# Kernel optimization log

Hardware: AMD Instinct MI355X
Metric: run time of the kernel (lower is better)

## Reference

```python
import jax, jax.numpy as jnp
import numpy as np

B, L, H, V, HALF = 128, 4096, 64, 64, 32
ALPHA = 0.95
LN_EPS = 1e-5


def _normalize(x):
    # torch F.normalize(dim=-1): x / max(||x||_2, 1e-12)
    n = jnp.linalg.norm(x, axis=-1, keepdims=True)
    return x / jnp.maximum(n, 1e-12)


def setup_inputs() -> dict:
    key = jax.random.key(0)
    ks = jax.random.split(key, 17)
    s = 0.05
    return {
        "seq": jax.random.randint(ks[0], (B, L), 0, V),
        "embed": jax.random.normal(ks[1], (V, H), jnp.float32),
        "W1": jax.random.normal(ks[2], (H, 2 * H), jnp.float32) * s,
        "b1": jnp.zeros((2 * H,), jnp.float32),
        "W2": jax.random.normal(ks[3], (2 * H, H), jnp.float32) * s,
        "b2": jnp.zeros((H,), jnp.float32),
        "gamma": jnp.ones((H,), jnp.float32),
        "beta": jnp.zeros((H,), jnp.float32),
        "Ws": jax.random.normal(ks[4], (H, HALF), jnp.float32) * s,
        "bs": jnp.zeros((HALF,), jnp.float32),
        "We": jax.random.normal(ks[5], (H, HALF), jnp.float32) * s,
        "be": jnp.zeros((HALF,), jnp.float32),
        "Wrp": jax.random.normal(ks[6], (2 * HALF, H), jnp.float32) * s,
        "brp": jnp.zeros((H,), jnp.float32),
        "Wout": jax.random.normal(ks[7], (H, V), jnp.float32) * s,
        "bout": jnp.zeros((V,), jnp.float32),
    }


def _forward(seq, embed, W1, b1, W2, b2, gamma, beta,
             Ws, bs, We, be, Wrp, brp, Wout, bout):
    # Encoder: embed + FF(ReLU) residual + LayerNorm
    h0 = embed[seq]                                   # [B,L,H]
    ff = jnp.maximum(h0 @ W1 + b1, 0.0) @ W2 + b2
    x = h0 + ff
    mu = x.mean(-1, keepdims=True)
    var = ((x - mu) ** 2).mean(-1, keepdims=True)
    h = (x - mu) / jnp.sqrt(var + LN_EPS) * gamma + beta  # [B,L,H]

    # Precompute per-step projections for t = 0 .. L-2
    hp = h[:, :-1, :]                                 # [B,L-1,H]
    hs = hp @ Ws + bs                                 # [B,L-1,HALF]
    he = hp @ We + be
    ksn = _normalize(hs)
    ken = _normalize(he)
    scale = (jnp.arange(L - 1, dtype=h.dtype) + 1.0) / L  # (t+1)/L

    def step(carry, inp):
        M_s, M_e = carry                              # [B,HALF,HALF]
        hs_t, he_t, ks_t, ke_t, sc = inp
        vps = jnp.einsum('bij,bj->bi', M_s, ks_t)
        vpe = jnp.einsum('bij,bj->bi', M_e, ke_t)
        M_s = M_s + (1.0 - ALPHA) * (hs_t - vps)[:, :, None] * ks_t[:, None, :]
        M_e = M_e + (1.0 - ALPHA) * sc * (he_t - vpe)[:, :, None] * ke_t[:, None, :]
        return (M_s, M_e), None

    xs = (jnp.swapaxes(hs, 0, 1), jnp.swapaxes(he, 0, 1),
          jnp.swapaxes(ksn, 0, 1), jnp.swapaxes(ken, 0, 1), scale)
    M0 = jnp.zeros((B, HALF, HALF), h.dtype)
    (M_s, M_e), _ = jax.lax.scan(step, (M0, M0), xs)

    # Read with last-token query
    q = h[:, -1, :]
    qs = _normalize(q @ Ws + bs)
    qe = _normalize(q @ We + be)
    rs = jnp.einsum('bij,bj->bi', M_s, qs)
    re = jnp.einsum('bij,bj->bi', M_e, qe)
    r = jnp.concatenate([rs, re], axis=-1)            # [B,2*HALF]
    return (r @ Wrp + brp) @ Wout + bout              # [B,V]


def reference(seq, embed, W1, b1, W2, b2, gamma, beta,
              Ws, bs, We, be, Wrp, brp, Wout, bout):
    return _forward(seq, embed, W1, b1, W2, b2, gamma, beta,
                    Ws, bs, We, be, Wrp, brp, Wout, bout)
```

## Files before the change

kernel.cpp:

```cpp
#include <hip/hip_runtime.h>
#include <hip/hip_bf16.h>
#include <stdint.h>


#define BETA 0.05f
#define NB 128
#define NL 4096
#define TC 16
#define NCH 256
#define NBLD 7
#define SLOT_F 1360
#define NSLOT 14

#define L_GR   (NSLOT * SLOT_F)
#define L_DA   (L_GR + 4096)
#define L_RV   (L_DA + 64)
#define L_O1   (L_RV + 64)
#define L_WHO  (L_O1 + 64)
#define L_TOT  (L_WHO + 1)

struct Ptrs { const void* p[15]; };

__device__ inline float readlane_f(float v, int l) {
    return __int_as_float(__builtin_amdgcn_readlane(__float_as_int(v), l));
}
__device__ inline float ldT(const float* p, int i) { return p[i]; }
__device__ inline float ldT(const __hip_bfloat16* p, int i) { return __bfloat162float(p[i]); }

template <typename T>
__device__ void build_tables_body(const T* emb, const T* W1, const T* b1,
                                  const T* W2, const T* b2, const T* gam,
                                  const T* bet, const T* Wsm, const T* bsv,
                                  const T* Wem, const T* bev, float* tbl)
{
    int v = blockIdx.x;
    int j = threadIdx.x;
    __shared__ float h0s[64];
    __shared__ float act[128];
    __shared__ float hrow[64];

    float h0 = ldT(emb, v * 64 + j);
    h0s[j] = h0;
    __syncthreads();

    float za = ldT(b1, j);
    float zb = ldT(b1, j + 64);
    for (int k = 0; k < 64; ++k) {
        float hk = h0s[k];
        za = fmaf(hk, ldT(W1, k * 128 + j), za);
        zb = fmaf(hk, ldT(W1, k * 128 + j + 64), zb);
    }
    act[j] = fmaxf(za, 0.0f);
    act[j + 64] = fmaxf(zb, 0.0f);
    __syncthreads();

    float ff = ldT(b2, j);
    for (int k = 0; k < 128; ++k)
        ff = fmaf(act[k], ldT(W2, k * 64 + j), ff);
    float x = h0 + ff;

    float s = x;
    for (int off = 32; off >= 1; off >>= 1) s += __shfl_xor(s, off, 64);
    float mu = s * (1.0f / 64.0f);
    float d = x - mu;
    float s2 = d * d;
    for (int off = 32; off >= 1; off >>= 1) s2 += __shfl_xor(s2, off, 64);
    float var = s2 * (1.0f / 64.0f);
    float h = d / sqrtf(var + 1e-5f) * ldT(gam, j) + ldT(bet, j);
    hrow[j] = h;
    __syncthreads();

    if (j < 32) {
        float sv = ldT(bsv, j);
        for (int k = 0; k < 64; ++k)
            sv = fmaf(hrow[k], ldT(Wsm, k * 32 + j), sv);
        float n2 = sv * sv;
        for (int off = 16; off >= 1; off >>= 1) n2 += __shfl_xor(n2, off, 64);
        float nrm = fmaxf(sqrtf(n2), 1e-12f);
        tbl[v * 32 + j] = sv;
        tbl[2048 + v * 32 + j] = sv / nrm;
    } else {
        int jj = j - 32;
        float ev = ldT(bev, jj);
        for (int k = 0; k < 64; ++k)
            ev = fmaf(hrow[k], ldT(Wem, k * 32 + jj), ev);
        float n2 = ev * ev;
        for (int off = 16; off >= 1; off >>= 1) n2 += __shfl_xor(n2, off, 64);
        float nrm = fmaxf(sqrtf(n2), 1e-12f);
        tbl[4096 + v * 32 + jj] = ev;
        tbl[6144 + v * 32 + jj] = ev / nrm;
    }
}

__global__ __launch_bounds__(64, 2) void build_tables(Ptrs ps, float* __restrict__ tbl,
                                                      int* __restrict__ flags)
{
    if (blockIdx.x == 0) {
        flags[threadIdx.x] = 0;
        flags[threadIdx.x + 64] = 0;
    }
    uint32_t g0 = *(const uint32_t*)ps.p[5];
    if (g0 == 0x3F803F80u)
        build_tables_body((const __hip_bfloat16*)ps.p[0], (const __hip_bfloat16*)ps.p[1],
                          (const __hip_bfloat16*)ps.p[2], (const __hip_bfloat16*)ps.p[3],
                          (const __hip_bfloat16*)ps.p[4], (const __hip_bfloat16*)ps.p[5],
                          (const __hip_bfloat16*)ps.p[6], (const __hip_bfloat16*)ps.p[7],
                          (const __hip_bfloat16*)ps.p[8], (const __hip_bfloat16*)ps.p[9],
                          (const __hip_bfloat16*)ps.p[10], tbl);
    else
        build_tables_body((const float*)ps.p[0], (const float*)ps.p[1],
                          (const float*)ps.p[2], (const float*)ps.p[3],
                          (const float*)ps.p[4], (const float*)ps.p[5],
                          (const float*)ps.p[6], (const float*)ps.p[7],
                          (const float*)ps.p[8], (const float*)ps.p[9],
                          (const float*)ps.p[10], tbl);
}

__global__ __launch_bounds__(512, 1) void ema_ms(
    const int* __restrict__ seq, const float* __restrict__ tbl,
    Ptrs ps, float* __restrict__ rvbuf, int* __restrict__ flags,
    void* __restrict__ outv)
{
    __shared__ float S[L_TOT];

    int bm = blockIdx.x;
    int b = bm >> 1, mat = bm & 1;
    int tid = threadIdx.x;
    int wid = tid >> 6, lane = tid & 63;
    const float bstep = BETA / 4096.0f;

    if (tid < 64) S[L_DA + tid] = 0.0f;

    const float* ktab = tbl + 2048 + mat * 4096;
    for (int i = tid; i < 2048; i += 512)
        S[(i >> 5) * 33 + (i & 31)] = ktab[i];
    __syncthreads();

    {
        float Kown[32];
#pragma unroll
        for (int j = 0; j < 32; ++j) Kown[j] = S[lane * 33 + j];
        for (int v8 = 0; v8 < 8; ++v8) {
            int vt = wid * 8 + v8;
            float acc = 0.0f;
#pragma unroll
            for (int j = 0; j < 32; ++j)
                acc = fmaf(S[vt * 33 + j], Kown[j], acc);
            S[L_GR + vt * 64 + lane] = acc;
        }
    }
    __syncthreads();

    const int* sb = seq + (size_t)b * NL;
    float y = 0.0f;
    if (wid == 0) {
        int vlast = sb[NL - 1];
        y = S[L_GR + vlast * 64 + lane];
    }

    const int NRND = (NCH + NBLD - 1) / NBLD;

    for (int r = 0; r <= NRND; ++r) {
        if (wid != 0) {
            int bi = wid - 1;
            int ci = NBLD * r + bi;
            if (r < NRND && ci < NCH) {
                int c = NCH - 1 - ci;
                float* slot = S + ((r & 1) * NBLD + bi) * SLOT_F;
                int tokv = 0; float bneg = 0.0f;
                if (lane < TC) {
                    int t = c * TC + (TC - 1) - lane;
                    tokv = sb[t];
                    float bb = mat ? bstep * (float)(t + 1) : BETA;
                    if (t == NL - 1) bb = 0.0f;
                    bneg = -bb;
                    ((int*)(slot + 1344))[lane] = tokv;
                }
                float garr[TC];
#pragma unroll
                for (int p = 0; p < TC; ++p) {
                    int vp = __builtin_amdgcn_readlane(tokv, p);
                    const float* gr = S + L_GR + vp * 64;
                    slot[320 + p * 64 + lane] = gr[lane];
                    garr[p] = gr[tokv] * bneg;
                }
                float x[TC];
                x[0] = (lane == 0) ? 1.0f : 0.0f;
#pragma unroll
                for (int p = 1; p < TC; ++p) {
                    float xp = (lane == p) ? 1.0f : 0.0f;
#pragma unroll
                    for (int j = 0; j < p; ++j)
                        xp = fmaf(readlane_f(garr[p], j), x[j], xp);
                    x[p] = xp;
                }
                if (lane < TC) {
#pragma unroll
                    for (int p = 0; p < TC; ++p)
                        slot[p * 20 + lane] = x[p];
                }
            }
        } else if (r >= 1) {
            int rpar = ((r - 1) & 1) * NBLD;
            int base_ci = NBLD * (r - 1);
            int nch_r = NCH - base_ci;
            if (nch_r > NBLD) nch_r = NBLD;

            float* slot0 = S + rpar * SLOT_F;
            int tokc = ((int*)(slot0 + 1344))[lane & 15];
            int stokc[16];
#pragma unroll
            for (int q = 0; q < 16; ++q)
                stokc[q] = __builtin_amdgcn_readlane(tokc, q);
            const float4* vr0 = (const float4*)(slot0 + (lane & 15) * 20);
            float4 Vc0 = vr0[0], Vc1 = vr0[1], Vc2 = vr0[2], Vc3 = vr0[3];
            float gpc[16];
#pragma unroll
            for (int p = 0; p < 16; ++p)
                gpc[p] = slot0[320 + p * 64 + lane];

            for (int bi = 0; bi < nch_r; ++bi) {
                int c = NCH - 1 - (base_ci + bi);

                int bin = (bi + 1 < nch_r) ? (bi + 1) : bi;
                float* slotn = S + (rpar + bin) * SLOT_F;
                int tokn = ((int*)(slotn + 1344))[lane & 15];
                int stokn[16];
#pragma unroll
                for (int q = 0; q < 16; ++q)
                    stokn[q] = __builtin_amdgcn_readlane(tokn, q);
                const float4* vrn = (const float4*)(slotn + (lane & 15) * 20);
                float4 Vn0 = vrn[0], Vn1 = vrn[1], Vn2 = vrn[2], Vn3 = vrn[3];
                float gpn[16];
#pragma unroll
                for (int p = 0; p < 16; ++p)
                    gpn[p] = slotn[320 + p * 64 + lane];
                asm volatile("" ::: "memory");

                float bv = 0.0f;
                if (lane < TC) {
                    int t = c * TC + (TC - 1) - lane;
                    float bb = mat ? bstep * (float)(t + 1) : BETA;
                    if (t == NL - 1) bb = 0.0f;
                    bv = bb;
                }
                float ryq[16];
#pragma unroll
                for (int q = 0; q < 16; ++q)
                    ryq[q] = readlane_f(y, stokc[q]);
                float s0 = Vc0.x * ryq[0];
                float s1 = Vc0.y * ryq[1];
                float s2 = Vc0.z * ryq[2];
                float s3 = Vc0.w * ryq[3];
                s0 = fmaf(Vc1.x, ryq[4], s0);
                s1 = fmaf(Vc1.y, ryq[5], s1);
                s2 = fmaf(Vc1.z, ryq[6], s2);
                s3 = fmaf(Vc1.w, ryq[7], s3);
                s0 = fmaf(Vc2.x, ryq[8], s0);
                s1 = fmaf(Vc2.y, ryq[9], s1);
                s2 = fmaf(Vc2.z, ryq[10], s2);
                s3 = fmaf(Vc2.w, ryq[11], s3);
                s0 = fmaf(Vc3.x, ryq[12], s0);
                s1 = fmaf(Vc3.y, ryq[13], s1);
                s2 = fmaf(Vc3.z, ryq[14], s2);
                s3 = fmaf(Vc3.w, ryq[15], s3);
                float dv = ((s0 + s1) + (s2 + s3)) * bv;
                float dn = -dv;
                float ya = 0.f, yb = 0.f, yc2 = 0.f, yd = 0.f;
#pragma unroll
                for (int p = 0; p < TC; p += 4) {
                    ya  = fmaf(readlane_f(dn, p),     gpc[p],     ya);
                    yb  = fmaf(readlane_f(dn, p + 1), gpc[p + 1], yb);
                    yc2 = fmaf(readlane_f(dn, p + 2), gpc[p + 2], yc2);
                    yd  = fmaf(readlane_f(dn, p + 3), gpc[p + 3], yd);
                }
                y += (ya + yb) + (yc2 + yd);
                if (lane < TC) atomicAdd(&S[L_DA + tokc], dv);

                tokc = tokn;
#pragma unroll
                for (int q = 0; q < 16; ++q) stokc[q] = stokn[q];
                Vc0 = Vn0; Vc1 = Vn1; Vc2 = Vn2; Vc3 = Vn3;
#pragma unroll
                for (int p = 0; p < 16; ++p) gpc[p] = gpn[p];
            }
        }
        __syncthreads();
    }

    if (tid < 32) {
        float rr = 0.0f;
        const float* hsrc = tbl + mat * 4096;
        for (int v = 0; v < 64; ++v)
            rr = fmaf(S[L_DA + v], hsrc[v * 32 + tid], rr);
        __hip_atomic_store(&rvbuf[bm * 32 + tid], rr,
                           __ATOMIC_RELAXED, __HIP_MEMORY_SCOPE_AGENT);
    }
    __syncthreads();
    if (tid == 0) {
        int old = __hip_atomic_fetch_add(&flags[b], 1,
                                         __ATOMIC_ACQ_REL, __HIP_MEMORY_SCOPE_AGENT);
        ((int*)S)[L_WHO] = old;
    }
    __syncthreads();
    if (((int*)S)[L_WHO] != 1) return;

    if (tid < 64)
        S[L_RV + tid] = __hip_atomic_load(&rvbuf[b * 64 + tid],
                                          __ATOMIC_RELAXED, __HIP_MEMORY_SCOPE_AGENT);
    __syncthreads();

    uint32_t g0h = *(const uint32_t*)ps.p[5];
    int isbf = (g0h == 0x3F803F80u) ? 1 : 0;
    if (tid < 64) {
        float o;
        if (isbf) {
            const __hip_bfloat16* W = (const __hip_bfloat16*)ps.p[11];
            o = __bfloat162float(((const __hip_bfloat16*)ps.p[12])[tid]);
            for (int i = 0; i < 64; ++i)
                o = fmaf(S[L_RV + i], __bfloat162float(W[i * 64 + tid]), o);
        } else {
            const float* W = (const float*)ps.p[11];
            o = ((const float*)ps.p[12])[tid];
            for (int i = 0; i < 64; ++i)
                o = fmaf(S[L_RV + i], W[i * 64 + tid], o);
        }
        S[L_O1 + tid] = o;
    }
    __syncthreads();
    if (tid < 64) {
        float o2;
        if (isbf) {
            const __hip_bfloat16* W = (const __hip_bfloat16*)ps.p[13];
            o2 = __bfloat162float(((const __hip_bfloat16*)ps.p[14])[tid]);
            for (int i = 0; i < 64; ++i)
                o2 = fmaf(S[L_O1 + i], __bfloat162float(W[i * 64 + tid]), o2);
            ((__hip_bfloat16*)outv)[b * 64 + tid] = __float2bfloat16(o2);
        } else {
            const float* W = (const float*)ps.p[13];
            o2 = ((const float*)ps.p[14])[tid];
            for (int i = 0; i < 64; ++i)
                o2 = fmaf(S[L_O1 + i], W[i * 64 + tid], o2);
            ((float*)outv)[b * 64 + tid] = o2;
        }
    }
}

extern "C" void kernel_launch(void* const* d_in, const int* in_sizes, int n_in,
                              void* d_out, int out_size, void* d_ws, size_t ws_size,
                              hipStream_t stream) {
    const int* seq = (const int*)d_in[0];
    Ptrs ps;
    for (int i = 0; i < 15; ++i) ps.p[i] = d_in[i + 1];

    float* tbl = (float*)d_ws;
    float* rvbuf = tbl + 8192;
    int* flags = (int*)(rvbuf + 8192);

    build_tables<<<64, 64, 0, stream>>>(ps, tbl, flags);
    ema_ms<<<NB * 2, 512, 0, stream>>>(seq, tbl, ps, rvbuf, flags, d_out);
}
```

Measured before the change: 213.6 us.

## Drop per-chunk Gram row copies, read Gram table directly, restructure chunk solve

Builder waves stop copying the 16 Gram rows per chunk into their slot. The consumer wave now reads those rows straight from the shared Gram table using the token indices, which shrinks each slot from 1360 to 336 floats. The triangular solve is rewritten as a backward recurrence that produces the transposed coefficient rows and stores them as float4. Builder count drops from 7 to 6, with wave 4 left idle, and the shared array is 16-byte aligned for the vector stores. The aim is to cut LDS traffic and footprint in the builder stage, at the cost of fewer builders per round and gather-style LDS reads in the serial consumer wave.

Measured after the change: 200.8 us. 1.06x faster.

```diff
diff --git a/kernel.cpp b/kernel.cpp
--- a/kernel.cpp
+++ b/kernel.cpp
@@ -8,9 +8,9 @@
 #define NL 4096
 #define TC 16
 #define NCH 256
-#define NBLD 7
-#define SLOT_F 1360
-#define NSLOT 14
+#define NBLD 6
+#define SLOT_F 336
+#define NSLOT 12
 
 #define L_GR   (NSLOT * SLOT_F)
 #define L_DA   (L_GR + 4096)
@@ -121,7 +121,7 @@
     Ptrs ps, float* __restrict__ rvbuf, int* __restrict__ flags,
     void* __restrict__ outv)
 {
-    __shared__ float S[L_TOT];
+    __shared__ __align__(16) float S[L_TOT];
 
     int bm = blockIdx.x;
     int b = bm >> 1, mat = bm & 1;
@@ -161,8 +161,8 @@
     const int NRND = (NCH + NBLD - 1) / NBLD;
 
     for (int r = 0; r <= NRND; ++r) {
-        if (wid != 0) {
-            int bi = wid - 1;
+        if (wid != 0 && wid != 4) {
+            int bi = (wid > 4) ? (wid - 2) : (wid - 1);
             int ci = NBLD * r + bi;
             if (r < NRND && ci < NCH) {
                 int c = NCH - 1 - ci;
@@ -174,40 +174,40 @@
                     float bb = mat ? bstep * (float)(t + 1) : BETA;
                     if (t == NL - 1) bb = 0.0f;
                     bneg = -bb;
-                    ((int*)(slot + 1344))[lane] = tokv;
+                    ((int*)(slot + 320))[lane] = tokv;
                 }
                 float garr[TC];
 #pragma unroll
                 for (int p = 0; p < TC; ++p) {
                     int vp = __builtin_amdgcn_readlane(tokv, p);
-                    const float* gr = S + L_GR + vp * 64;
-                    slot[320 + p * 64 + lane] = gr[lane];
-                    garr[p] = gr[tokv] * bneg;
-                }
-                float x[TC];
-                x[0] = (lane == 0) ? 1.0f : 0.0f;
-#pragma unroll
-                for (int p = 1; p < TC; ++p) {
-                    float xp = (lane == p) ? 1.0f : 0.0f;
-#pragma unroll
-                    for (int j = 0; j < p; ++j)
-                        xp = fmaf(readlane_f(garr[p], j), x[j], xp);
-                    x[p] = xp;
+                    garr[p] = S[L_GR + vp * 64 + tokv] * bneg;
+                }
+                float z[TC];
+                z[15] = (lane == 15) ? 1.0f : 0.0f;
+#pragma unroll
+                for (int q = TC - 2; q >= 0; --q) {
+                    float zq = (lane == q) ? 1.0f : 0.0f;
+#pragma unroll
+                    for (int j = q + 1; j < TC; ++j)
+                        zq = fmaf(readlane_f(garr[j], q), z[j], zq);
+                    z[q] = zq;
                 }
                 if (lane < TC) {
-#pragma unroll
-                    for (int p = 0; p < TC; ++p)
-                        slot[p * 20 + lane] = x[p];
+                    float4* vd = (float4*)(slot + lane * 20);
+                    vd[0] = make_float4(z[0], z[1], z[2], z[3]);
+                    vd[1] = make_float4(z[4], z[5], z[6], z[7]);
+                    vd[2] = make_float4(z[8], z[9], z[10], z[11]);
+                    vd[3] = make_float4(z[12], z[13], z[14], z[15]);
                 }
             }
-        } else if (r >= 1) {
+        } else if (wid == 0 && r >= 1) {
             int rpar = ((r - 1) & 1) * NBLD;
             int base_ci = NBLD * (r - 1);
             int nch_r = NCH - base_ci;
             if (nch_r > NBLD) nch_r = NBLD;
 
             float* slot0 = S + rpar * SLOT_F;
-            int tokc = ((int*)(slot0 + 1344))[lane & 15];
+            int tokc = ((int*)(slot0 + 320))[lane & 15];
             int stokc[16];
 #pragma unroll
             for (int q = 0; q < 16; ++q)
@@ -217,14 +217,14 @@
             float gpc[16];
 #pragma unroll
             for (int p = 0; p < 16; ++p)
-                gpc[p] = slot0[320 + p * 64 + lane];
+                gpc[p] = S[L_GR + stokc[p] * 64 + lane];
 
             for (int bi = 0; bi < nch_r; ++bi) {
                 int c = NCH - 1 - (base_ci + bi);
 
                 int bin = (bi + 1 < nch_r) ? (bi + 1) : bi;
                 float* slotn = S + (rpar + bin) * SLOT_F;
-                int tokn = ((int*)(slotn + 1344))[lane & 15];
+                int tokn = ((int*)(slotn + 320))[lane & 15];
                 int stokn[16];
 #pragma unroll
                 for (int q = 0; q < 16; ++q)
@@ -234,7 +234,7 @@
                 float gpn[16];
 #pragma unroll
                 for (int p = 0; p < 16; ++p)
-                    gpn[p] = slotn[320 + p * 64 + lane];
+                    gpn[p] = S[L_GR + stokn[p] * 64 + lane];
                 asm volatile("" ::: "memory");
 
                 float bv = 0.0f;
```
